# Optimization experiments

Measured on AMD Instinct MI355X. Metric: run time of the kernel, lower is better.

## Reference

```python
import jax, jax.numpy as jnp
import numpy as np

L = 24        # n_layer
E = 1024      # n_emb
H = 4 * E     # ffn hidden
V = 50277     # vocab
LN_EPS = 1e-5


def _ln(x, w, b):
    m = x.mean(-1, keepdims=True)
    v = ((x - m) ** 2).mean(-1, keepdims=True)
    return (x - m) / jnp.sqrt(v + LN_EPS) * w + b


def setup_inputs() -> dict:
    key = jax.random.key(0)
    ks = jax.random.split(key, 24)
    s = 1.0 / np.sqrt(E)      # keep matvec outputs O(1) so exp-recurrence is stable
    sh = 1.0 / np.sqrt(H)
    inp = {
        "emb":      jax.random.normal(ks[0], (V, E), jnp.float32) * 0.02,
        "ln0_w":    jnp.ones((E,), jnp.float32),
        "ln0_b":    jnp.zeros((E,), jnp.float32),
        "ln1_w":    jnp.ones((L, E), jnp.float32),
        "ln1_b":    jnp.zeros((L, E), jnp.float32),
        "att_tmk":  jax.random.uniform(ks[1], (L, E), jnp.float32),
        "att_tmv":  jax.random.uniform(ks[2], (L, E), jnp.float32),
        "att_tmr":  jax.random.uniform(ks[3], (L, E), jnp.float32),
        "att_tf":   jax.random.normal(ks[4], (L, E), jnp.float32) * 0.3,
        # checkpoint stores raw time_decay; loader applies -exp(.)
        "att_td":   -jnp.exp(jax.random.normal(ks[5], (L, E), jnp.float32) * 0.3),
        "att_kw":   jax.random.normal(ks[6], (L, E, E), jnp.float32) * s,
        "att_vw":   jax.random.normal(ks[7], (L, E, E), jnp.float32) * s,
        "att_rw":   jax.random.normal(ks[8], (L, E, E), jnp.float32) * s,
        "att_ow":   jax.random.normal(ks[9], (L, E, E), jnp.float32) * s,
        "ln2_w":    jnp.ones((L, E), jnp.float32),
        "ln2_b":    jnp.zeros((L, E), jnp.float32),
        "ffn_tmk":  jax.random.uniform(ks[10], (L, E), jnp.float32),
        "ffn_tmr":  jax.random.uniform(ks[11], (L, E), jnp.float32),
        "ffn_kw":   jax.random.normal(ks[12], (L, H, E), jnp.float32) * s,
        "ffn_vw":   jax.random.normal(ks[13], (L, E, H), jnp.float32) * sh,
        "ffn_rw":   jax.random.normal(ks[14], (L, E, E), jnp.float32) * s,
        "ln_out_w": jnp.ones((E,), jnp.float32),
        "ln_out_b": jnp.zeros((E,), jnp.float32),
        "head_w":   jax.random.normal(ks[15], (V, E), jnp.float32) * s,
        "token":    123,
    }
    state = jnp.zeros((5 * L, E), jnp.float32)
    state = state.at[4::5].set(-1e30)  # pp slot, as in empty_state()
    inp["state"] = state
    return inp


def _rwkv_forward(emb, ln0_w, ln0_b, ln1_w, ln1_b, att_tmk, att_tmv, att_tmr,
                  att_tf, att_td, att_kw, att_vw, att_rw, att_ow,
                  ln2_w, ln2_b, ffn_tmk, ffn_tmr, ffn_kw, ffn_vw, ffn_rw,
                  ln_out_w, ln_out_b, head_w, state, token):
    x = emb[token]
    x = _ln(x, ln0_w, ln0_b)           # blocks.0.ln0 applied once before layer 0
    st = state.reshape(L, 5, E)        # slots: (ffn_x, att_x, aa, bb, pp)

    def step(x, inp):
        (s, l1w, l1b, tmk, tmv, tmr, tf, td, kw, vw, rw, ow,
         l2w, l2b, ftmk, ftmr, fkw, fvw, frw) = inp
        ffn_x, att_x, aa, bb, pp = s[0], s[1], s[2], s[3], s[4]
        # --- time-mix (SA) ---
        xn = _ln(x, l1w, l1b)
        xk = xn * tmk + att_x * (1 - tmk)
        xv = xn * tmv + att_x * (1 - tmv)
        xr = xn * tmr + att_x * (1 - tmr)
        r = jax.nn.sigmoid(rw @ xr)
        k = kw @ xk
        v = vw @ xv
        # numerically-stabilized WKV output
        ww = tf + k
        p = jnp.maximum(pp, ww)
        e1 = jnp.exp(pp - p)
        e2 = jnp.exp(ww - p)
        a = e1 * aa + e2 * v
        b = e1 * bb + e2
        # state update
        ww2 = pp + td
        p2 = jnp.maximum(ww2, k)
        f1 = jnp.exp(ww2 - p2)
        f2 = jnp.exp(k - p2)
        naa = f1 * aa + f2 * v
        nbb = f1 * bb + f2
        npp = p2
        sx = x + ow @ (r * a / b)
        # --- channel-mix (FF) ---
        xn2 = _ln(sx, l2w, l2b)
        fxk = xn2 * ftmk + ffn_x * (1 - ftmk)
        fxr = xn2 * ftmr + ffn_x * (1 - ftmr)
        fr = jax.nn.sigmoid(frw @ fxr)
        fk = jnp.square(jax.nn.relu(fkw @ fxk))
        out = sx + fr * (fvw @ fk)
        new_s = jnp.stack([xn2, xn, naa, nbb, npp])
        return out, new_s

    xs = (st, ln1_w, ln1_b, att_tmk, att_tmv, att_tmr, att_tf, att_td,
          att_kw, att_vw, att_rw, att_ow, ln2_w, ln2_b, ffn_tmk, ffn_tmr,
          ffn_kw, ffn_vw, ffn_rw)
    x, new_st = jax.lax.scan(step, x, xs)
    logits = head_w @ _ln(x, ln_out_w, ln_out_b)
    return logits, new_st.reshape(5 * L, E)


def reference(emb, ln0_w, ln0_b, ln1_w, ln1_b, att_tmk, att_tmv, att_tmr,
              att_tf, att_td, att_kw, att_vw, att_rw, att_ow,
              ln2_w, ln2_b, ffn_tmk, ffn_tmr, ffn_kw, ffn_vw, ffn_rw,
              ln_out_w, ln_out_b, head_w, state, token):
    return _rwkv_forward(emb, ln0_w, ln0_b, ln1_w, ln1_b, att_tmk, att_tmv,
                         att_tmr, att_tf, att_td, att_kw, att_vw, att_rw,
                         att_ow, ln2_w, ln2_b, ffn_tmk, ffn_tmr, ffn_kw,
                         ffn_vw, ffn_rw, ln_out_w, ln_out_b, head_w,
                         state, token)
```

## Files before the change

### kernel.cpp

```cpp
#include <hip/hip_runtime.h>

#define E 1024
#define H 4096
#define NLAYER 24
#define V 50277
#define NB 256
#define NT 1024
#define LN_EPS 1e-5f

typedef unsigned long long u64;

#define R1O    0
#define R2O    16384
#define POOLO  32768
#define SXO    36864
#define SSXO   37888
#define FXRO   38912
#define REDO   39936
#define PARTO  39968
#define PART2O 39984
#define SMEMF  40000

struct Params {
  const float* emb;   const float* ln0_w; const float* ln0_b;
  const float* ln1_w; const float* ln1_b;
  const float* tmk;   const float* tmv;   const float* tmr;
  const float* tf;    const float* td;
  const float* kw;    const float* vw;    const float* rw;  const float* ow;
  const float* ln2_w; const float* ln2_b;
  const float* ftmk;  const float* ftmr;
  const float* fkw;   const float* fvw;   const float* frw;
  const float* lnow;  const float* lnob;  const float* headw;
  const float* st;    const int* tok;
  float* out; float* ws;
};

__device__ __forceinline__ void stg_tag(u64* p, float v, unsigned tag) {
  u64 w = ((u64)__float_as_uint(v) << 32) | (u64)tag;
  __hip_atomic_store(p, w, __ATOMIC_RELAXED, __HIP_MEMORY_SCOPE_AGENT);
}
__device__ __forceinline__ u64 ld_tag(const u64* p) {
  return __hip_atomic_load(p, __ATOMIC_RELAXED, __HIP_MEMORY_SCOPE_AGENT);
}
__device__ __forceinline__ float poll_tag(const u64* p, unsigned tag) {
  u64 w = ld_tag(p);
  while ((unsigned)w != tag) { __builtin_amdgcn_s_sleep(1); w = ld_tag(p); }
  return __uint_as_float((unsigned)(w >> 32));
}

__device__ __forceinline__ void wait_pf() {
  asm volatile("s_waitcnt vmcnt(0)" ::: "memory");
}

__device__ __forceinline__ void gload_lds16(const float* g, float* l) {
  __builtin_amdgcn_global_load_lds(
      (const __attribute__((address_space(1))) unsigned int*)(g),
      (__attribute__((address_space(3))) unsigned int*)(l), 16, 0, 0);
}
__device__ __forceinline__ void pf_row4k(const float* row, float* dst, int lane) {
#pragma unroll
  for (int c = 0; c < 4; ++c)
    gload_lds16(row + c * 256 + lane * 4, dst + c * 256);
}

__device__ __forceinline__ float warp_sum(float v) {
#pragma unroll
  for (int off = 32; off; off >>= 1) v += __shfl_down(v, off);
  return v;
}

__device__ __forceinline__ float2 ln_stats(float v, float* red) {
  float a = v, b = v * v;
#pragma unroll
  for (int off = 32; off; off >>= 1) { a += __shfl_xor(a, off); b += __shfl_xor(b, off); }
  const int wid = threadIdx.x >> 6, lane = threadIdx.x & 63;
  if (lane == 0) { red[2 * wid] = a; red[2 * wid + 1] = b; }
  __syncthreads();
  float s1 = 0.f, s2 = 0.f;
  const float2* r2 = (const float2*)red;
#pragma unroll
  for (int j = 0; j < 16; ++j) { float2 t = r2[j]; s1 += t.x; s2 += t.y; }
  float m = s1 * (1.f / E);
  return make_float2(m, s2 * (1.f / E) - m * m);
}

__device__ __forceinline__ float dot4(float4 a, float4 b) {
  return a.x * b.x + a.y * b.y + a.z * b.z + a.w * b.w;
}

__device__ __forceinline__ float dotlds(const float* wrow, const float* vec, int lane) {
  const float4* w4 = (const float4*)wrow;
  const float4* v4 = (const float4*)vec;
  float acc = 0.f;
#pragma unroll
  for (int p = 0; p < 4; ++p)
    acc += dot4(w4[lane + p * 64], v4[lane + p * 64]);
  return warp_sum(acc);
}

__global__ __launch_bounds__(NT, 1) void rwkv_kernel(Params p) {
  const int tid = threadIdx.x, bid = blockIdx.x;
  const int lane = tid & 63, wid = tid >> 6;

  extern __shared__ float smem[];
  float* r1     = smem + R1O;
  float* r2     = smem + R2O;
  float* pool   = smem + POOLO;
  float* s_x    = smem + SXO;
  float* s_sx   = smem + SSXO;
  float* s_fxr  = smem + FXRO;
  float* s_red  = smem + REDO;
  float* s_part = smem + PARTO;
  float* s_part2= smem + PART2O;

  u64* tws = (u64*)p.ws;
  u64* tk  = tws;
  u64* tv  = tws + 2 * E;
  u64* tr  = tws + 4 * E;
  u64* tsx = tws + 6 * E;
  u64* tx  = tws + 8 * E;
  u64* tfk = tws + 10 * E;

  float* out_st = p.out + V;
  const int token = p.tok[0];

  const bool hasA = wid < 12;
  const int rA = bid * 12 + wid;
  const int matA = rA >> 10, rmA = rA & (E - 1);
  const int rloc = wid >> 2, kc = wid & 3;
  const int rowO = bid * 4 + rloc;
  float* wA = r1 + wid * 1024;
  float* wD = r2 + rloc * 4096 + kc * 1024;

  if (hasA) {
    const float* W = (matA == 0 ? p.kw : matA == 1 ? p.vw : p.rw) + (size_t)rmA * E;
    pf_row4k(W, wA, lane);
  }

  {
    float v = p.emb[(size_t)token * E + tid];
    float2 mv = ln_stats(v, s_red);
    s_x[tid] = (v - mv.x) / sqrtf(mv.y + LN_EPS) * p.ln0_w[tid] + p.ln0_b[tid];
  }

  for (int l = 0; l < NLAYER; ++l) {
    const float* stl = p.st + (size_t)5 * l * E;
    float* ostl = out_st + (size_t)5 * l * E;
    const int par = l & 1;
    const unsigned tg = (unsigned)(l + 1);

    float l1w = p.ln1_w[l * E + tid], l1b = p.ln1_b[l * E + tid];
    float ax = stl[E + tid];
    float ta = p.tmk[l * E + tid], tb = p.tmv[l * E + tid], tc = p.tmr[l * E + tid];
    float xv_;
    if (l > 0) { xv_ = poll_tag(&tx[par * E + tid], (unsigned)l); s_x[tid] = xv_; }
    else       { xv_ = s_x[tid]; }
    {
      float2 mv = ln_stats(xv_, s_red);
      float xn = (xv_ - mv.x) / sqrtf(mv.y + LN_EPS) * l1w + l1b;
      pool[tid]        = xn * ta + ax * (1.f - ta);
      pool[1024 + tid] = xn * tb + ax * (1.f - tb);
      pool[2048 + tid] = xn * tc + ax * (1.f - tc);
      if (bid == 0) ostl[E + tid] = xn;
    }
    __syncthreads();
    wait_pf();
    if (hasA) {
      float d = dotlds(wA, pool + matA * 1024, lane);
      if (lane == 0) {
        u64* dst = (matA == 0 ? tk : matA == 1 ? tv : tr) + par * E + rmA;
        stg_tag(dst, matA == 2 ? 1.f / (1.f + expf(-d)) : d, tg);
      }
    }

    {
      float aav = stl[2 * E + tid], bbv = stl[3 * E + tid], ppv = stl[4 * E + tid];
      float tfv = p.tf[l * E + tid], tdv = p.td[l * E + tid];
      float4 wow = ((const float4*)(p.ow + (size_t)l * E * E + (size_t)rowO * E + kc * 256))[lane];
      pf_row4k(p.fkw + (size_t)l * H * E + (size_t)(bid * 16 + wid) * E, wA, lane);
      const u64 *bk = tk + par * E + tid, *bv = tv + par * E + tid, *br = tr + par * E + tid;
      u64 wk = ld_tag(bk), wv = ld_tag(bv), wr = ld_tag(br);
      while ((unsigned)wk != tg) { __builtin_amdgcn_s_sleep(1); wk = ld_tag(bk); }
      while ((unsigned)wv != tg) { __builtin_amdgcn_s_sleep(1); wv = ld_tag(bv); }
      while ((unsigned)wr != tg) { __builtin_amdgcn_s_sleep(1); wr = ld_tag(br); }
      float kk = __uint_as_float((unsigned)(wk >> 32));
      float vv = __uint_as_float((unsigned)(wv >> 32));
      float rr = __uint_as_float((unsigned)(wr >> 32));
      float wwv = tfv + kk;
      float pm = fmaxf(ppv, wwv);
      float e1 = expf(ppv - pm), e2 = expf(wwv - pm);
      float a = e1 * aav + e2 * vv, b = e1 * bbv + e2;
      pool[3072 + tid] = rr * a / b;
      float ww2 = ppv + tdv;
      float p2 = fmaxf(ww2, kk);
      float f1 = expf(ww2 - p2), f2 = expf(kk - p2);
      if (bid == 0) {
        ostl[2 * E + tid] = f1 * aav + f2 * vv;
        ostl[3 * E + tid] = f1 * bbv + f2;
        ostl[4 * E + tid] = p2;
      }
      __syncthreads();
      const float4* v4 = (const float4*)(pool + 3072 + kc * 256);
      float acc = warp_sum(dot4(wow, v4[lane]));
      if (lane == 0) s_part[wid] = acc;
    }
    __syncthreads();
    if (tid < 4) {
      float dsum = s_part[tid * 4] + s_part[tid * 4 + 1] +
                   s_part[tid * 4 + 2] + s_part[tid * 4 + 3];
      stg_tag(&tsx[par * E + bid * 4 + tid], s_x[bid * 4 + tid] + dsum, tg);
    }

    {
      float l2w = p.ln2_w[l * E + tid], l2b = p.ln2_b[l * E + tid];
      float fx = stl[tid];
      float fa = p.ftmk[l * E + tid], fb = p.ftmr[l * E + tid];
      float4 wfr = ((const float4*)(p.frw + (size_t)l * E * E + (size_t)rowO * E + kc * 256))[lane];
      pf_row4k(p.fvw + (size_t)l * E * H + (size_t)rowO * H + kc * 1024, wD, lane);
      float sxv = poll_tag(&tsx[par * E + tid], tg);
      s_sx[tid] = sxv;
      float2 mv = ln_stats(sxv, s_red);
      float xn2 = (sxv - mv.x) / sqrtf(mv.y + LN_EPS) * l2w + l2b;
      pool[tid]  = xn2 * fa + fx * (1.f - fa);
      s_fxr[tid] = xn2 * fb + fx * (1.f - fb);
      if (bid == 0) ostl[tid] = xn2;
      __syncthreads();
      float d = dotlds(wA, pool, lane);
      if (lane == 0) { float t = fmaxf(d, 0.f); stg_tag(&tfk[par * H + bid * 16 + wid], t * t, tg); }
      const float4* f4 = (const float4*)(s_fxr + kc * 256);
      float fp = warp_sum(dot4(wfr, f4[lane]));
      if (lane == 0) s_part2[wid] = fp;
    }

    if (l + 1 < NLAYER && hasA) {
      const float* W = (matA == 0 ? p.kw : matA == 1 ? p.vw : p.rw) +
                       (size_t)(l + 1) * E * E + (size_t)rmA * E;
      pf_row4k(W, wA, lane);
    }
    __syncthreads();
    {
      const u64* base = tfk + par * H;
      u64 w0 = ld_tag(base + tid);
      u64 w1 = ld_tag(base + tid + 1024);
      u64 w2 = ld_tag(base + tid + 2048);
      u64 w3 = ld_tag(base + tid + 3072);
      while ((unsigned)w0 != tg) { __builtin_amdgcn_s_sleep(1); w0 = ld_tag(base + tid); }
      while ((unsigned)w1 != tg) { __builtin_amdgcn_s_sleep(1); w1 = ld_tag(base + tid + 1024); }
      while ((unsigned)w2 != tg) { __builtin_amdgcn_s_sleep(1); w2 = ld_tag(base + tid + 2048); }
      while ((unsigned)w3 != tg) { __builtin_amdgcn_s_sleep(1); w3 = ld_tag(base + tid + 3072); }
      pool[tid]        = __uint_as_float((unsigned)(w0 >> 32));
      pool[tid + 1024] = __uint_as_float((unsigned)(w1 >> 32));
      pool[tid + 2048] = __uint_as_float((unsigned)(w2 >> 32));
      pool[tid + 3072] = __uint_as_float((unsigned)(w3 >> 32));
    }
    __syncthreads();
    {
      const float4* v4 = (const float4*)(pool + kc * 1024);
      const float4* w4 = (const float4*)wD;
      float acc = 0.f;
#pragma unroll
      for (int pc = 0; pc < 4; ++pc)
        acc += dot4(w4[lane + pc * 64], v4[lane + pc * 64]);
      acc = warp_sum(acc);
      if (lane == 0) s_part[wid] = acc;
    }
    __syncthreads();
    if (tid < 4) {
      float dsum = s_part[tid * 4] + s_part[tid * 4 + 1] +
                   s_part[tid * 4 + 2] + s_part[tid * 4 + 3];
      float frs  = s_part2[tid * 4] + s_part2[tid * 4 + 1] +
                   s_part2[tid * 4 + 2] + s_part2[tid * 4 + 3];
      float fr = 1.f / (1.f + expf(-frs));
      stg_tag(&tx[((l + 1) & 1) * E + bid * 4 + tid],
              s_sx[bid * 4 + tid] + fr * dsum, tg);
    }
  }

  {
    float xv_ = poll_tag(&tx[(NLAYER & 1) * E + tid], (unsigned)NLAYER);
    float2 mv = ln_stats(xv_, s_red);
    pool[tid] = (xv_ - mv.x) / sqrtf(mv.y + LN_EPS) * p.lnow[tid] + p.lnob[tid];
  }
  __syncthreads();
  {
    const int gw = bid * 16 + wid;
    const float4* v4 = (const float4*)pool;
    float4 x0 = v4[lane], x1 = v4[lane + 64], x2 = v4[lane + 128], x3 = v4[lane + 192];
    int row = gw;
    for (; row + 12288 < V; row += 16384) {
      const float4* W0 = (const float4*)(p.headw + (size_t)row * E);
      const float4* W1 = (const float4*)(p.headw + (size_t)(row + 4096) * E);
      const float4* W2 = (const float4*)(p.headw + (size_t)(row + 8192) * E);
      const float4* W3 = (const float4*)(p.headw + (size_t)(row + 12288) * E);
      float a0 = 0.f, a1 = 0.f, a2 = 0.f, a3 = 0.f;
      a0 += dot4(W0[lane], x0) + dot4(W0[lane + 64], x1) + dot4(W0[lane + 128], x2) + dot4(W0[lane + 192], x3);
      a1 += dot4(W1[lane], x0) + dot4(W1[lane + 64], x1) + dot4(W1[lane + 128], x2) + dot4(W1[lane + 192], x3);
      a2 += dot4(W2[lane], x0) + dot4(W2[lane + 64], x1) + dot4(W2[lane + 128], x2) + dot4(W2[lane + 192], x3);
      a3 += dot4(W3[lane], x0) + dot4(W3[lane + 64], x1) + dot4(W3[lane + 128], x2) + dot4(W3[lane + 192], x3);
      a0 = warp_sum(a0); a1 = warp_sum(a1); a2 = warp_sum(a2); a3 = warp_sum(a3);
      if (lane == 0) {
        p.out[row] = a0; p.out[row + 4096] = a1;
        p.out[row + 8192] = a2; p.out[row + 12288] = a3;
      }
    }
    for (; row < V; row += 4096) {
      const float4* W0 = (const float4*)(p.headw + (size_t)row * E);
      float a0 = dot4(W0[lane], x0) + dot4(W0[lane + 64], x1) +
                 dot4(W0[lane + 128], x2) + dot4(W0[lane + 192], x3);
      a0 = warp_sum(a0);
      if (lane == 0) p.out[row] = a0;
    }
  }
}

extern "C" void kernel_launch(void* const* d_in, const int* in_sizes, int n_in,
                              void* d_out, int out_size, void* d_ws, size_t ws_size,
                              hipStream_t stream) {
  Params p;
  p.emb   = (const float*)d_in[0];
  p.ln0_w = (const float*)d_in[1];
  p.ln0_b = (const float*)d_in[2];
  p.ln1_w = (const float*)d_in[3];
  p.ln1_b = (const float*)d_in[4];
  p.tmk   = (const float*)d_in[5];
  p.tmv   = (const float*)d_in[6];
  p.tmr   = (const float*)d_in[7];
  p.tf    = (const float*)d_in[8];
  p.td    = (const float*)d_in[9];
  p.kw    = (const float*)d_in[10];
  p.vw    = (const float*)d_in[11];
  p.rw    = (const float*)d_in[12];
  p.ow    = (const float*)d_in[13];
  p.ln2_w = (const float*)d_in[14];
  p.ln2_b = (const float*)d_in[15];
  p.ftmk  = (const float*)d_in[16];
  p.ftmr  = (const float*)d_in[17];
  p.fkw   = (const float*)d_in[18];
  p.fvw   = (const float*)d_in[19];
  p.frw   = (const float*)d_in[20];
  p.lnow  = (const float*)d_in[21];
  p.lnob  = (const float*)d_in[22];
  p.headw = (const float*)d_in[23];
  if (in_sizes[24] == 1) {
    p.tok = (const int*)d_in[24];
    p.st  = (const float*)d_in[25];
  } else {
    p.st  = (const float*)d_in[24];
    p.tok = (const int*)d_in[25];
  }
  p.out   = (float*)d_out;
  p.ws    = (float*)d_ws;

  hipMemsetAsync(d_ws, 0, (10 * E + 2 * H) * sizeof(unsigned long long), stream);

  void* args[] = { &p };
  hipLaunchCooperativeKernel((const void*)rwkv_kernel, dim3(NB), dim3(NT),
                             args, SMEMF * sizeof(float), stream);
}
```

Measured before the change: 550.2 us.

## Dedicate four polling waves per block and remap compute waves to twelve

Splits each block into 12 compute waves and 4 dedicated polling/elementwise waves. The polling waves handle tag waits, layernorms and the WKV recurrence, each over four elements per thread, while the compute waves issue weight prefetches and matvecs. Compute waves take over the rows formerly owned by waves 12-15. Syncs become raw s_barrier with lgkmcnt waits, and the full vmcnt(0) waits become partial vmcnt counts so prefetches stay in flight. This aims to overlap weight streaming with the cross-block wait latency, at the cost of uneven per-wave work and fragile vmcnt accounting.

```diff
diff --git a/kernel.cpp b/kernel.cpp
--- a/kernel.cpp
+++ b/kernel.cpp
@@ -15,11 +15,10 @@
 #define POOLO  32768
 #define SXO    36864
 #define SSXO   37888
-#define FXRO   38912
-#define REDO   39936
-#define PARTO  39968
-#define PART2O 39984
-#define SMEMF  40000
+#define REDO   38912
+#define PARTO  38944
+#define PART2O 38960
+#define SMEMF  38976
 
 struct Params {
   const float* emb;   const float* ln0_w; const float* ln0_b;
@@ -42,14 +41,18 @@
 __device__ __forceinline__ u64 ld_tag(const u64* p) {
   return __hip_atomic_load(p, __ATOMIC_RELAXED, __HIP_MEMORY_SCOPE_AGENT);
 }
-__device__ __forceinline__ float poll_tag(const u64* p, unsigned tag) {
-  u64 w = ld_tag(p);
-  while ((unsigned)w != tag) { __builtin_amdgcn_s_sleep(1); w = ld_tag(p); }
+#define TAGWAIT(w, ptr, tagv) \
+  while ((unsigned)(w) != (tagv)) { __builtin_amdgcn_s_sleep(1); (w) = ld_tag(ptr); }
+__device__ __forceinline__ float tagval(u64 w) {
   return __uint_as_float((unsigned)(w >> 32));
 }
 
-__device__ __forceinline__ void wait_pf() {
-  asm volatile("s_waitcnt vmcnt(0)" ::: "memory");
+#define WAITVM(N) asm volatile("s_waitcnt vmcnt(" #N ")" ::: "memory")
+
+__device__ __forceinline__ void bar() {
+  asm volatile("s_waitcnt lgkmcnt(0)" ::: "memory");
+  __builtin_amdgcn_s_barrier();
+  asm volatile("" ::: "memory");
 }
 
 __device__ __forceinline__ void gload_lds16(const float* g, float* l) {
@@ -69,7 +72,21 @@
   return v;
 }
 
-__device__ __forceinline__ float2 ln_stats(float v, float* red) {
+__device__ __forceinline__ float dot4(float4 a, float4 b) {
+  return a.x * b.x + a.y * b.y + a.z * b.z + a.w * b.w;
+}
+
+__device__ __forceinline__ float dotlds(const float* wrow, const float* vec, int lane) {
+  const float4* w4 = (const float4*)wrow;
+  const float4* v4 = (const float4*)vec;
+  float acc = 0.f;
+#pragma unroll
+  for (int p = 0; p < 4; ++p)
+    acc += dot4(w4[lane + p * 64], v4[lane + p * 64]);
+  return warp_sum(acc);
+}
+
+__device__ __forceinline__ float2 ln_stats_w16(float v, float* red) {
   float a = v, b = v * v;
 #pragma unroll
   for (int off = 32; off; off >>= 1) { a += __shfl_xor(a, off); b += __shfl_xor(b, off); }
@@ -84,20 +101,6 @@
   return make_float2(m, s2 * (1.f / E) - m * m);
 }
 
-__device__ __forceinline__ float dot4(float4 a, float4 b) {
-  return a.x * b.x + a.y * b.y + a.z * b.z + a.w * b.w;
-}
-
-__device__ __forceinline__ float dotlds(const float* wrow, const float* vec, int lane) {
-  const float4* w4 = (const float4*)wrow;
-  const float4* v4 = (const float4*)vec;
-  float acc = 0.f;
-#pragma unroll
-  for (int p = 0; p < 4; ++p)
-    acc += dot4(w4[lane + p * 64], v4[lane + p * 64]);
-  return warp_sum(acc);
-}
-
 __global__ __launch_bounds__(NT, 1) void rwkv_kernel(Params p) {
   const int tid = threadIdx.x, bid = blockIdx.x;
   const int lane = tid & 63, wid = tid >> 6;
@@ -108,7 +111,6 @@
   float* pool   = smem + POOLO;
   float* s_x    = smem + SXO;
   float* s_sx   = smem + SSXO;
-  float* s_fxr  = smem + FXRO;
   float* s_red  = smem + REDO;
   float* s_part = smem + PARTO;
   float* s_part2= smem + PART2O;
@@ -124,24 +126,25 @@
   float* out_st = p.out + V;
   const int token = p.tok[0];
 
-  const bool hasA = wid < 12;
+  const bool isPol = wid >= 12;
+  const int pw = wid - 12;
+  const int pt = tid - 768;
+
   const int rA = bid * 12 + wid;
   const int matA = rA >> 10, rmA = rA & (E - 1);
-  const int rloc = wid >> 2, kc = wid & 3;
-  const int rowO = bid * 4 + rloc;
   float* wA = r1 + wid * 1024;
-  float* wD = r2 + rloc * 4096 + kc * 1024;
-
-  if (hasA) {
+
+  if (!isPol) {
     const float* W = (matA == 0 ? p.kw : matA == 1 ? p.vw : p.rw) + (size_t)rmA * E;
     pf_row4k(W, wA, lane);
   }
 
   {
     float v = p.emb[(size_t)token * E + tid];
-    float2 mv = ln_stats(v, s_red);
+    float2 mv = ln_stats_w16(v, s_red);
     s_x[tid] = (v - mv.x) / sqrtf(mv.y + LN_EPS) * p.ln0_w[tid] + p.ln0_b[tid];
   }
+  __syncthreads();
 
   for (int l = 0; l < NLAYER; ++l) {
     const float* stl = p.st + (size_t)5 * l * E;
@@ -149,23 +152,51 @@
     const int par = l & 1;
     const unsigned tg = (unsigned)(l + 1);
 
-    float l1w = p.ln1_w[l * E + tid], l1b = p.ln1_b[l * E + tid];
-    float ax = stl[E + tid];
-    float ta = p.tmk[l * E + tid], tb = p.tmv[l * E + tid], tc = p.tmr[l * E + tid];
-    float xv_;
-    if (l > 0) { xv_ = poll_tag(&tx[par * E + tid], (unsigned)l); s_x[tid] = xv_; }
-    else       { xv_ = s_x[tid]; }
-    {
-      float2 mv = ln_stats(xv_, s_red);
-      float xn = (xv_ - mv.x) / sqrtf(mv.y + LN_EPS) * l1w + l1b;
-      pool[tid]        = xn * ta + ax * (1.f - ta);
-      pool[1024 + tid] = xn * tb + ax * (1.f - tb);
-      pool[2048 + tid] = xn * tc + ax * (1.f - tc);
-      if (bid == 0) ostl[E + tid] = xn;
-    }
-    __syncthreads();
-    wait_pf();
-    if (hasA) {
+    float xv0, xv1, xv2, xv3;
+    float a0[4], a1[4], a2[4], a3[4], a4[4], a5[4];
+    if (isPol) {
+#pragma unroll
+      for (int i = 0; i < 4; ++i) { int e = pt + (i << 8);
+        a0[i] = p.ln1_w[l * E + e]; a1[i] = p.ln1_b[l * E + e];
+        a2[i] = stl[E + e];
+        a3[i] = p.tmk[l * E + e]; a4[i] = p.tmv[l * E + e]; a5[i] = p.tmr[l * E + e];
+      }
+      if (l > 0) {
+        const u64* b = tx + par * E;
+        u64 q0 = ld_tag(b + pt), q1 = ld_tag(b + pt + 256);
+        u64 q2 = ld_tag(b + pt + 512), q3 = ld_tag(b + pt + 768);
+        TAGWAIT(q0, b + pt, (unsigned)l);       TAGWAIT(q1, b + pt + 256, (unsigned)l);
+        TAGWAIT(q2, b + pt + 512, (unsigned)l); TAGWAIT(q3, b + pt + 768, (unsigned)l);
+        xv0 = tagval(q0); xv1 = tagval(q1); xv2 = tagval(q2); xv3 = tagval(q3);
+        s_x[pt] = xv0; s_x[pt + 256] = xv1; s_x[pt + 512] = xv2; s_x[pt + 768] = xv3;
+      } else {
+        xv0 = s_x[pt]; xv1 = s_x[pt + 256]; xv2 = s_x[pt + 512]; xv3 = s_x[pt + 768];
+      }
+      float sa = xv0 + xv1 + xv2 + xv3;
+      float sb = xv0 * xv0 + xv1 * xv1 + xv2 * xv2 + xv3 * xv3;
+#pragma unroll
+      for (int off = 32; off; off >>= 1) { sa += __shfl_xor(sa, off); sb += __shfl_xor(sb, off); }
+      if (lane == 0) { s_red[2 * pw] = sa; s_red[2 * pw + 1] = sb; }
+    }
+    bar();
+    if (isPol) {
+      float s1 = s_red[0] + s_red[2] + s_red[4] + s_red[6];
+      float s2 = s_red[1] + s_red[3] + s_red[5] + s_red[7];
+      float m = s1 * (1.f / E), var = s2 * (1.f / E) - m * m;
+      float is = 1.f / sqrtf(var + LN_EPS);
+      float xvv[4] = { xv0, xv1, xv2, xv3 };
+#pragma unroll
+      for (int i = 0; i < 4; ++i) { int e = pt + (i << 8);
+        float xn = (xvv[i] - m) * is * a0[i] + a1[i];
+        pool[e]        = xn * a3[i] + a2[i] * (1.f - a3[i]);
+        pool[1024 + e] = xn * a4[i] + a2[i] * (1.f - a4[i]);
+        pool[2048 + e] = xn * a5[i] + a2[i] * (1.f - a5[i]);
+        if (bid == 0) ostl[E + e] = xn;
+      }
+    }
+    bar();
+    if (!isPol) {
+      WAITVM(0);
       float d = dotlds(wA, pool + matA * 1024, lane);
       if (lane == 0) {
         u64* dst = (matA == 0 ? tk : matA == 1 ? tv : tr) + par * E + rmA;
@@ -173,98 +204,176 @@
       }
     }
 
-    {
-      float aav = stl[2 * E + tid], bbv = stl[3 * E + tid], ppv = stl[4 * E + tid];
-      float tfv = p.tf[l * E + tid], tdv = p.td[l * E + tid];
-      float4 wow = ((const float4*)(p.ow + (size_t)l * E * E + (size_t)rowO * E + kc * 256))[lane];
+    float4 wow0, wow1;
+    if (!isPol) {
+      { int c = wid;
+        wow0 = ((const float4*)(p.ow + (size_t)l * E * E +
+                 (size_t)(bid * 4 + (c >> 2)) * E + (c & 3) * 256))[lane]; }
+      if (wid < 4) { int c = 12 + wid;
+        wow1 = ((const float4*)(p.ow + (size_t)l * E * E +
+                 (size_t)(bid * 4 + (c >> 2)) * E + (c & 3) * 256))[lane]; }
       pf_row4k(p.fkw + (size_t)l * H * E + (size_t)(bid * 16 + wid) * E, wA, lane);
-      const u64 *bk = tk + par * E + tid, *bv = tv + par * E + tid, *br = tr + par * E + tid;
-      u64 wk = ld_tag(bk), wv = ld_tag(bv), wr = ld_tag(br);
-      while ((unsigned)wk != tg) { __builtin_amdgcn_s_sleep(1); wk = ld_tag(bk); }
-      while ((unsigned)wv != tg) { __builtin_amdgcn_s_sleep(1); wv = ld_tag(bv); }
-      while ((unsigned)wr != tg) { __builtin_amdgcn_s_sleep(1); wr = ld_tag(br); }
-      float kk = __uint_as_float((unsigned)(wk >> 32));
-      float vv = __uint_as_float((unsigned)(wv >> 32));
-      float rr = __uint_as_float((unsigned)(wr >> 32));
-      float wwv = tfv + kk;
-      float pm = fmaxf(ppv, wwv);
-      float e1 = expf(ppv - pm), e2 = expf(wwv - pm);
-      float a = e1 * aav + e2 * vv, b = e1 * bbv + e2;
-      pool[3072 + tid] = rr * a / b;
-      float ww2 = ppv + tdv;
-      float p2 = fmaxf(ww2, kk);
-      float f1 = expf(ww2 - p2), f2 = expf(kk - p2);
-      if (bid == 0) {
-        ostl[2 * E + tid] = f1 * aav + f2 * vv;
-        ostl[3 * E + tid] = f1 * bbv + f2;
-        ostl[4 * E + tid] = p2;
-      }
-      __syncthreads();
-      const float4* v4 = (const float4*)(pool + 3072 + kc * 256);
-      float acc = warp_sum(dot4(wow, v4[lane]));
+      if (wid < 4)
+        pf_row4k(p.fkw + (size_t)l * H * E + (size_t)(bid * 16 + 12 + wid) * E,
+                 r1 + (12 + wid) * 1024, lane);
+    } else {
+      float wa[4], wb[4], wp[4], wf[4], wd[4];
+#pragma unroll
+      for (int i = 0; i < 4; ++i) { int e = pt + (i << 8);
+        wa[i] = stl[2 * E + e]; wb[i] = stl[3 * E + e]; wp[i] = stl[4 * E + e];
+        wf[i] = p.tf[l * E + e]; wd[i] = p.td[l * E + e];
+      }
+#pragma unroll
+      for (int i = 0; i < 4; ++i) { int e = pt + (i << 8);
+        const u64 *pk = &tk[par * E + e], *pv = &tv[par * E + e], *pr = &tr[par * E + e];
+        u64 qk = ld_tag(pk), qv = ld_tag(pv), qr = ld_tag(pr);
+        TAGWAIT(qk, pk, tg); TAGWAIT(qv, pv, tg); TAGWAIT(qr, pr, tg);
+        float kk = tagval(qk), vv = tagval(qv), rr = tagval(qr);
+        float wwv = wf[i] + kk;
+        float pm = fmaxf(wp[i], wwv);
+        float e1 = expf(wp[i] - pm), e2 = expf(wwv - pm);
+        float aa = e1 * wa[i] + e2 * vv, bb = e1 * wb[i] + e2;
+        pool[3072 + e] = rr * aa / bb;
+        float ww2 = wp[i] + wd[i];
+        float p2 = fmaxf(ww2, kk);
+        float f1 = expf(ww2 - p2), f2 = expf(kk - p2);
+        if (bid == 0) {
+          ostl[2 * E + e] = f1 * wa[i] + f2 * vv;
+          ostl[3 * E + e] = f1 * wb[i] + f2;
+          ostl[4 * E + e] = p2;
+        }
+      }
+    }
+    bar();
+    if (!isPol) {
+      const float4* v4 = (const float4*)(pool + 3072 + (wid & 3) * 256);
+      float acc = warp_sum(dot4(wow0, v4[lane]));
       if (lane == 0) s_part[wid] = acc;
-    }
-    __syncthreads();
+      if (wid < 4) {
+        float acc2 = warp_sum(dot4(wow1, v4[lane]));
+        if (lane == 0) s_part[12 + wid] = acc2;
+      }
+    }
+    bar();
     if (tid < 4) {
       float dsum = s_part[tid * 4] + s_part[tid * 4 + 1] +
                    s_part[tid * 4 + 2] + s_part[tid * 4 + 3];
       stg_tag(&tsx[par * E + bid * 4 + tid], s_x[bid * 4 + tid] + dsum, tg);
     }
 
-    {
-      float l2w = p.ln2_w[l * E + tid], l2b = p.ln2_b[l * E + tid];
-      float fx = stl[tid];
-      float fa = p.ftmk[l * E + tid], fb = p.ftmr[l * E + tid];
-      float4 wfr = ((const float4*)(p.frw + (size_t)l * E * E + (size_t)rowO * E + kc * 256))[lane];
-      pf_row4k(p.fvw + (size_t)l * E * H + (size_t)rowO * H + kc * 1024, wD, lane);
-      float sxv = poll_tag(&tsx[par * E + tid], tg);
-      s_sx[tid] = sxv;
-      float2 mv = ln_stats(sxv, s_red);
-      float xn2 = (sxv - mv.x) / sqrtf(mv.y + LN_EPS) * l2w + l2b;
-      pool[tid]  = xn2 * fa + fx * (1.f - fa);
-      s_fxr[tid] = xn2 * fb + fx * (1.f - fb);
-      if (bid == 0) ostl[tid] = xn2;
-      __syncthreads();
+    float4 wfr0, wfr1;
+    float sx0, sx1, sx2, sx3;
+    float c0[4], c1[4], c2[4], c3[4], c4[4];
+    if (!isPol) {
+      { int c = wid;
+        wfr0 = ((const float4*)(p.frw + (size_t)l * E * E +
+                 (size_t)(bid * 4 + (c >> 2)) * E + (c & 3) * 256))[lane]; }
+      if (wid >= 4 && wid < 8) { int c = 8 + wid;
+        wfr1 = ((const float4*)(p.frw + (size_t)l * E * E +
+                 (size_t)(bid * 4 + (c >> 2)) * E + (c & 3) * 256))[lane]; }
+      { int c = wid;
+        pf_row4k(p.fvw + (size_t)l * E * H + (size_t)(bid * 4 + (c >> 2)) * H + (c & 3) * 1024,
+                 r2 + c * 1024, lane); }
+      if (wid >= 8) { int c = 4 + wid;
+        pf_row4k(p.fvw + (size_t)l * E * H + (size_t)(bid * 4 + (c >> 2)) * H + (c & 3) * 1024,
+                 r2 + c * 1024, lane); }
+    } else {
+#pragma unroll
+      for (int i = 0; i < 4; ++i) { int e = pt + (i << 8);
+        c0[i] = p.ln2_w[l * E + e]; c1[i] = p.ln2_b[l * E + e];
+        c2[i] = stl[e]; c3[i] = p.ftmk[l * E + e]; c4[i] = p.ftmr[l * E + e];
+      }
+      const u64* b = tsx + par * E;
+      u64 q0 = ld_tag(b + pt), q1 = ld_tag(b + pt + 256);
+      u64 q2 = ld_tag(b + pt + 512), q3 = ld_tag(b + pt + 768);
+      TAGWAIT(q0, b + pt, tg);       TAGWAIT(q1, b + pt + 256, tg);
+      TAGWAIT(q2, b + pt + 512, tg); TAGWAIT(q3, b + pt + 768, tg);
+      sx0 = tagval(q0); sx1 = tagval(q1); sx2 = tagval(q2); sx3 = tagval(q3);
+      s_sx[pt] = sx0; s_sx[pt + 256] = sx1; s_sx[pt + 512] = sx2; s_sx[pt + 768] = sx3;
+      float sa = sx0 + sx1 + sx2 + sx3;
+      float sb = sx0 * sx0 + sx1 * sx1 + sx2 * sx2 + sx3 * sx3;
+#pragma unroll
+      for (int off = 32; off; off >>= 1) { sa += __shfl_xor(sa, off); sb += __shfl_xor(sb, off); }
+      if (lane == 0) { s_red[2 * pw] = sa; s_red[2 * pw + 1] = sb; }
+    }
+    bar();
+    if (isPol) {
+      float s1 = s_red[0] + s_red[2] + s_red[4] + s_red[6];
+      float s2 = s_red[1] + s_red[3] + s_red[5] + s_red[7];
+      float m = s1 * (1.f / E), var = s2 * (1.f / E) - m * m;
+      float is = 1.f / sqrtf(var + LN_EPS);
+      float sxv[4] = { sx0, sx1, sx2, sx3 };
+#pragma unroll
+      for (int i = 0; i < 4; ++i) { int e = pt + (i << 8);
+        float xn2 = (sxv[i] - m) * is * c0[i] + c1[i];
+        pool[e]        = xn2 * c3[i] + c2[i] * (1.f - c3[i]);
+        pool[1024 + e] = xn2 * c4[i] + c2[i] * (1.f - c4[i]);
+        if (bid == 0) ostl[e] = xn2;
+      }
+    }
+    bar();
+    if (!isPol) {
+      if (wid < 4)      { WAITVM(5); }
+      else if (wid < 8) { WAITVM(6); }
+      else              { WAITVM(9); }
       float d = dotlds(wA, pool, lane);
       if (lane == 0) { float t = fmaxf(d, 0.f); stg_tag(&tfk[par * H + bid * 16 + wid], t * t, tg); }
-      const float4* f4 = (const float4*)(s_fxr + kc * 256);
-      float fp = warp_sum(dot4(wfr, f4[lane]));
+      if (wid < 4) {
+        float d2 = dotlds(r1 + (12 + wid) * 1024, pool, lane);
+        if (lane == 0) { float t = fmaxf(d2, 0.f); stg_tag(&tfk[par * H + bid * 16 + 12 + wid], t * t, tg); }
+      }
+      const float4* f4 = (const float4*)(pool + 1024 + (wid & 3) * 256);
+      float fp = warp_sum(dot4(wfr0, f4[lane]));
       if (lane == 0) s_part2[wid] = fp;
-    }
-
-    if (l + 1 < NLAYER && hasA) {
-      const float* W = (matA == 0 ? p.kw : matA == 1 ? p.vw : p.rw) +
-                       (size_t)(l + 1) * E * E + (size_t)rmA * E;
-      pf_row4k(W, wA, lane);
-    }
-    __syncthreads();
-    {
+      if (wid >= 4 && wid < 8) {
+        float fp2 = warp_sum(dot4(wfr1, f4[lane]));
+        if (lane == 0) s_part2[8 + wid] = fp2;
+      }
+    }
+    bar();
+
+    if (!isPol) {
+      if (l + 1 < NLAYER) {
+        const float* W = (matA == 0 ? p.kw : matA == 1 ? p.vw : p.rw) +
+                         (size_t)(l + 1) * E * E + (size_t)rmA * E;
+        pf_row4k(W, wA, lane);
+      }
+    } else {
       const u64* base = tfk + par * H;
-      u64 w0 = ld_tag(base + tid);
-      u64 w1 = ld_tag(base + tid + 1024);
-      u64 w2 = ld_tag(base + tid + 2048);
-      u64 w3 = ld_tag(base + tid + 3072);
-      while ((unsigned)w0 != tg) { __builtin_amdgcn_s_sleep(1); w0 = ld_tag(base + tid); }
-      while ((unsigned)w1 != tg) { __builtin_amdgcn_s_sleep(1); w1 = ld_tag(base + tid + 1024); }
-      while ((unsigned)w2 != tg) { __builtin_amdgcn_s_sleep(1); w2 = ld_tag(base + tid + 2048); }
-      while ((unsigned)w3 != tg) { __builtin_amdgcn_s_sleep(1); w3 = ld_tag(base + tid + 3072); }
-      pool[tid]        = __uint_as_float((unsigned)(w0 >> 32));
-      pool[tid + 1024] = __uint_as_float((unsigned)(w1 >> 32));
-      pool[tid + 2048] = __uint_as_float((unsigned)(w2 >> 32));
-      pool[tid + 3072] = __uint_as_float((unsigned)(w3 >> 32));
-    }
-    __syncthreads();
-    {
-      const float4* v4 = (const float4*)(pool + kc * 1024);
-      const float4* w4 = (const float4*)wD;
-      float acc = 0.f;
-#pragma unroll
-      for (int pc = 0; pc < 4; ++pc)
-        acc += dot4(w4[lane + pc * 64], v4[lane + pc * 64]);
-      acc = warp_sum(acc);
-      if (lane == 0) s_part[wid] = acc;
-    }
-    __syncthreads();
+#pragma unroll
+      for (int g = 0; g < 4; ++g) {
+        int o = pt + g * 1024;
+        u64 q0 = ld_tag(base + o), q1 = ld_tag(base + o + 256);
+        u64 q2 = ld_tag(base + o + 512), q3 = ld_tag(base + o + 768);
+        TAGWAIT(q0, base + o, tg);       TAGWAIT(q1, base + o + 256, tg);
+        TAGWAIT(q2, base + o + 512, tg); TAGWAIT(q3, base + o + 768, tg);
+        pool[o] = tagval(q0); pool[o + 256] = tagval(q1);
+        pool[o + 512] = tagval(q2); pool[o + 768] = tagval(q3);
+      }
+    }
+    bar();
+    if (!isPol) {
+      if (l + 1 < NLAYER) { WAITVM(4); } else { WAITVM(0); }
+      { int c = wid;
+        const float4* w4 = (const float4*)(r2 + c * 1024);
+        const float4* v4 = (const float4*)(pool + (c & 3) * 1024);
+        float acc = 0.f;
+#pragma unroll
+        for (int pc = 0; pc < 4; ++pc)
+          acc += dot4(w4[lane + pc * 64], v4[lane + pc * 64]);
+        acc = warp_sum(acc);
+        if (lane == 0) s_part[c] = acc; }
+      if (wid >= 8) { int c = 4 + wid;
+        const float4* w4 = (const float4*)(r2 + c * 1024);
+        const float4* v4 = (const float4*)(pool + (c & 3) * 1024);
+        float acc = 0.f;
+#pragma unroll
+        for (int pc = 0; pc < 4; ++pc)
+          acc += dot4(w4[lane + pc * 64], v4[lane + pc * 64]);
+        acc = warp_sum(acc);
+        if (lane == 0) s_part[c] = acc; }
+    }
+    bar();
     if (tid < 4) {
       float dsum = s_part[tid * 4] + s_part[tid * 4 + 1] +
                    s_part[tid * 4 + 2] + s_part[tid * 4 + 3];
@@ -277,11 +386,39 @@
   }
 
   {
-    float xv_ = poll_tag(&tx[(NLAYER & 1) * E + tid], (unsigned)NLAYER);
-    float2 mv = ln_stats(xv_, s_red);
-    pool[tid] = (xv_ - mv.x) / sqrtf(mv.y + LN_EPS) * p.lnow[tid] + p.lnob[tid];
-  }
-  __syncthreads();
+    float hx0, hx1, hx2, hx3;
+    float hw[4], hb[4];
+    if (isPol) {
+#pragma unroll
+      for (int i = 0; i < 4; ++i) { int e = pt + (i << 8);
+        hw[i] = p.lnow[e]; hb[i] = p.lnob[e];
+      }
+      const u64* b = tx + (NLAYER & 1) * E;
+      u64 q0 = ld_tag(b + pt), q1 = ld_tag(b + pt + 256);
+      u64 q2 = ld_tag(b + pt + 512), q3 = ld_tag(b + pt + 768);
+      TAGWAIT(q0, b + pt, (unsigned)NLAYER);       TAGWAIT(q1, b + pt + 256, (unsigned)NLAYER);
+      TAGWAIT(q2, b + pt + 512, (unsigned)NLAYER); TAGWAIT(q3, b + pt + 768, (unsigned)NLAYER);
+      hx0 = tagval(q0); hx1 = tagval(q1); hx2 = tagval(q2); hx3 = tagval(q3);
+      float sa = hx0 + hx1 + hx2 + hx3;
+      float sb = hx0 * hx0 + hx1 * hx1 + hx2 * hx2 + hx3 * hx3;
+#pragma unroll
+      for (int off = 32; off; off >>= 1) { sa += __shfl_xor(sa, off); sb += __shfl_xor(sb, off); }
+      if (lane == 0) { s_red[2 * pw] = sa; s_red[2 * pw + 1] = sb; }
+    }
+    bar();
+    if (isPol) {
+      float s1 = s_red[0] + s_red[2] + s_red[4] + s_red[6];
+      float s2 = s_red[1] + s_red[3] + s_red[5] + s_red[7];
+      float m = s1 * (1.f / E), var = s2 * (1.f / E) - m * m;
+      float is = 1.f / sqrtf(var + LN_EPS);
+      float hxv[4] = { hx0, hx1, hx2, hx3 };
+#pragma unroll
+      for (int i = 0; i < 4; ++i) { int e = pt + (i << 8);
+        pool[e] = (hxv[i] - m) * is * hw[i] + hb[i];
+      }
+    }
+    bar();
+  }
   {
     const int gw = bid * 16 + wid;
     const float4* v4 = (const float4*)pool;
```

Result: slower. 864.0 us (+57.0%).

## Co-locate k/v/r rows per block and compute WKV locally before one exchange

Applied to the files above, without the earlier changes.

Each block now computes the k, v and r rows for the same four embedding indices, so the WKV recurrence for those elements is computed locally from shared memory. Only the final rwkv output is published to global memory. This replaces three global tagged exchanges (k, v, r) with one, which cuts cross-block polling traffic and latency in the attention step. State writes are spread across blocks instead of done by block 0, and the small WKV computation now runs on only four threads per block.

```diff
diff --git a/kernel.cpp b/kernel.cpp
--- a/kernel.cpp
+++ b/kernel.cpp
@@ -114,9 +114,7 @@
   float* s_part2= smem + PART2O;
 
   u64* tws = (u64*)p.ws;
-  u64* tk  = tws;
-  u64* tv  = tws + 2 * E;
-  u64* tr  = tws + 4 * E;
+  u64* twk = tws;
   u64* tsx = tws + 6 * E;
   u64* tx  = tws + 8 * E;
   u64* tfk = tws + 10 * E;
@@ -125,15 +123,15 @@
   const int token = p.tok[0];
 
   const bool hasA = wid < 12;
-  const int rA = bid * 12 + wid;
-  const int matA = rA >> 10, rmA = rA & (E - 1);
+  const int matA = wid >> 2;
+  const int rowA = bid * 4 + (wid & 3);
   const int rloc = wid >> 2, kc = wid & 3;
   const int rowO = bid * 4 + rloc;
   float* wA = r1 + wid * 1024;
   float* wD = r2 + rloc * 4096 + kc * 1024;
 
   if (hasA) {
-    const float* W = (matA == 0 ? p.kw : matA == 1 ? p.vw : p.rw) + (size_t)rmA * E;
+    const float* W = (matA == 0 ? p.kw : matA == 1 ? p.vw : p.rw) + (size_t)rowA * E;
     pf_row4k(W, wA, lane);
   }
 
@@ -152,6 +150,12 @@
     float l1w = p.ln1_w[l * E + tid], l1b = p.ln1_b[l * E + tid];
     float ax = stl[E + tid];
     float ta = p.tmk[l * E + tid], tb = p.tmv[l * E + tid], tc = p.tmr[l * E + tid];
+    float aav, bbv, ppv, tfv, tdv;
+    const int eOwn = bid * 4 + tid;
+    if (tid < 4) {
+      aav = stl[2 * E + eOwn]; bbv = stl[3 * E + eOwn]; ppv = stl[4 * E + eOwn];
+      tfv = p.tf[l * E + eOwn]; tdv = p.td[l * E + eOwn];
+    }
     float xv_;
     if (l > 0) { xv_ = poll_tag(&tx[par * E + tid], (unsigned)l); s_x[tid] = xv_; }
     else       { xv_ = s_x[tid]; }
@@ -167,38 +171,29 @@
     wait_pf();
     if (hasA) {
       float d = dotlds(wA, pool + matA * 1024, lane);
-      if (lane == 0) {
-        u64* dst = (matA == 0 ? tk : matA == 1 ? tv : tr) + par * E + rmA;
-        stg_tag(dst, matA == 2 ? 1.f / (1.f + expf(-d)) : d, tg);
-      }
-    }
-
-    {
-      float aav = stl[2 * E + tid], bbv = stl[3 * E + tid], ppv = stl[4 * E + tid];
-      float tfv = p.tf[l * E + tid], tdv = p.td[l * E + tid];
-      float4 wow = ((const float4*)(p.ow + (size_t)l * E * E + (size_t)rowO * E + kc * 256))[lane];
-      pf_row4k(p.fkw + (size_t)l * H * E + (size_t)(bid * 16 + wid) * E, wA, lane);
-      const u64 *bk = tk + par * E + tid, *bv = tv + par * E + tid, *br = tr + par * E + tid;
-      u64 wk = ld_tag(bk), wv = ld_tag(bv), wr = ld_tag(br);
-      while ((unsigned)wk != tg) { __builtin_amdgcn_s_sleep(1); wk = ld_tag(bk); }
-      while ((unsigned)wv != tg) { __builtin_amdgcn_s_sleep(1); wv = ld_tag(bv); }
-      while ((unsigned)wr != tg) { __builtin_amdgcn_s_sleep(1); wr = ld_tag(br); }
-      float kk = __uint_as_float((unsigned)(wk >> 32));
-      float vv = __uint_as_float((unsigned)(wv >> 32));
-      float rr = __uint_as_float((unsigned)(wr >> 32));
+      if (lane == 0) s_part[wid] = d;
+    }
+    __syncthreads();
+    if (tid < 4) {
+      float kk = s_part[tid], vv = s_part[4 + tid];
+      float rr = 1.f / (1.f + expf(-s_part[8 + tid]));
       float wwv = tfv + kk;
       float pm = fmaxf(ppv, wwv);
       float e1 = expf(ppv - pm), e2 = expf(wwv - pm);
       float a = e1 * aav + e2 * vv, b = e1 * bbv + e2;
-      pool[3072 + tid] = rr * a / b;
+      stg_tag(&twk[par * E + eOwn], rr * a / b, tg);
       float ww2 = ppv + tdv;
       float p2 = fmaxf(ww2, kk);
       float f1 = expf(ww2 - p2), f2 = expf(kk - p2);
-      if (bid == 0) {
-        ostl[2 * E + tid] = f1 * aav + f2 * vv;
-        ostl[3 * E + tid] = f1 * bbv + f2;
-        ostl[4 * E + tid] = p2;
-      }
+      ostl[2 * E + eOwn] = f1 * aav + f2 * vv;
+      ostl[3 * E + eOwn] = f1 * bbv + f2;
+      ostl[4 * E + eOwn] = p2;
+    }
+
+    {
+      float4 wow = ((const float4*)(p.ow + (size_t)l * E * E + (size_t)rowO * E + kc * 256))[lane];
+      pf_row4k(p.fkw + (size_t)l * H * E + (size_t)(bid * 16 + wid) * E, wA, lane);
+      pool[3072 + tid] = poll_tag(&twk[par * E + tid], tg);
       __syncthreads();
       const float4* v4 = (const float4*)(pool + 3072 + kc * 256);
       float acc = warp_sum(dot4(wow, v4[lane]));
@@ -234,7 +229,7 @@
 
     if (l + 1 < NLAYER && hasA) {
       const float* W = (matA == 0 ? p.kw : matA == 1 ? p.vw : p.rw) +
-                       (size_t)(l + 1) * E * E + (size_t)rmA * E;
+                       (size_t)(l + 1) * E * E + (size_t)rowA * E;
       pf_row4k(W, wA, lane);
     }
     __syncthreads();
```

Measured after the change: 487.9 us (median of 2 runs). 11.3% less time.
